# Kernel tuning notes

Hardware: AMD Instinct MI355X
Metric: run time of the kernel (lower is better)

Reference implementation:

```python
import jax, jax.numpy as jnp
import numpy as np

N_NODES = 16384   # total nodes
B = 32            # graphs in batch
NPG = 512         # nodes per graph (uniform -> dense mask is all True)
E = 262144        # edges (avg degree 16)
H = 64            # hidden_dim
HEADS = 8
DH = H // HEADS


def setup_inputs() -> dict:
    key = jax.random.key(0)
    ks = jax.random.split(key, 20)
    x = jax.random.normal(ks[0], (N_NODES, H), dtype=jnp.float32)
    # edges constrained within each graph of 512 nodes
    src = jax.random.randint(ks[1], (E,), 0, N_NODES, dtype=jnp.int32)
    dst = (src // NPG) * NPG + jax.random.randint(ks[2], (E,), 0, NPG, dtype=jnp.int32)
    edge_index = jnp.stack([src, dst])
    batch = (jnp.arange(N_NODES, dtype=jnp.int32) // NPG)
    c_size = jnp.full((B,), NPG, dtype=jnp.int32)
    s = 1.0 / np.sqrt(H)
    p = lambda k, shape: (jax.random.normal(k, shape, dtype=jnp.float32) * s)
    return {
        "x": x,
        "w_gat": p(ks[3], (H, H)), "att_src": p(ks[4], (H,)), "att_dst": p(ks[5], (H,)), "b_gat": jnp.zeros((H,), jnp.float32),
        "g1": jnp.ones((H,), jnp.float32), "b1": jnp.zeros((H,), jnp.float32),
        "wq": p(ks[6], (H, H)), "bq": jnp.zeros((H,), jnp.float32),
        "wk": p(ks[7], (H, H)), "bk": jnp.zeros((H,), jnp.float32),
        "wv": p(ks[8], (H, H)), "bv": jnp.zeros((H,), jnp.float32),
        "wo": p(ks[9], (H, H)), "bo": jnp.zeros((H,), jnp.float32),
        "g2": jnp.ones((H,), jnp.float32), "b2": jnp.zeros((H,), jnp.float32),
        "edge_index": edge_index, "batch": batch, "c_size": c_size,
    }


def _layer_norm(x, g, b):
    mu = jnp.mean(x, axis=-1, keepdims=True)
    var = jnp.var(x, axis=-1, keepdims=True)
    return (x - mu) * jax.lax.rsqrt(var + 1e-5) * g + b


def _gat_conv(x, edge_index, w, a_src, a_dst, bias):
    # PyG GATConv, 1 head, add_self_loops=True, leaky_relu slope 0.2
    n = x.shape[0]
    loops = jnp.arange(n, dtype=edge_index.dtype)
    src = jnp.concatenate([edge_index[0], loops])
    dst = jnp.concatenate([edge_index[1], loops])
    h = x @ w                                  # [n, H]
    e = jax.nn.leaky_relu((h @ a_src)[src] + (h @ a_dst)[dst], 0.2)  # [E+n]
    m = jax.ops.segment_max(e, dst, num_segments=n)
    p = jnp.exp(e - m[dst])
    s = jax.ops.segment_sum(p, dst, num_segments=n)
    alpha = p / (s[dst] + 1e-16)
    out = jax.ops.segment_sum(alpha[:, None] * h[src], dst, num_segments=n)
    return out + bias


def reference(x, w_gat, att_src, att_dst, b_gat, g1, b1,
              wq, bq, wk, bk, wv, bv, wo, bo, g2, b2,
              edge_index, batch, c_size):
    # GAT branch (dropout is identity in eval)
    x_ = jax.nn.relu(_gat_conv(x, edge_index, w_gat, att_src, att_dst, b_gat))
    x1 = _layer_norm(x + x_, g1, b1)                     # [n, H]
    # to_dense_batch: uniform graphs -> mask all True, plain reshape
    xd = x1.reshape(B, NPG, H)
    q = (xd @ wq + bq).reshape(B, NPG, HEADS, DH)
    k = (xd @ wk + bk).reshape(B, NPG, HEADS, DH)
    v = (xd @ wv + bv).reshape(B, NPG, HEADS, DH)
    scores = jnp.einsum('bqhd,bkhd->bhqk', q, k) / np.sqrt(DH)  # [B,h,N,N]
    attn = jax.nn.softmax(scores, axis=-1)
    o = jnp.einsum('bhqk,bkhd->bqhd', attn, v).reshape(B, NPG, H)
    o = o @ wo + bo
    x2 = _layer_norm(x1 + jax.nn.relu(o.reshape(N_NODES, H)), g2, b2)
    return x2  # recon_loss is None in eval mode
```

## Files before the change

### kernel.cpp

```cpp
#include <hip/hip_runtime.h>
#include <hip/hip_bf16.h>

#define NN     16384
#define HD     64
#define BG     32
#define NPG    512
#define NHEADS 8
#define DH     8
#define DEGMAX 40

#define KVSTR  20
#define CSTR   (64 * KVSTR + 4)
#define QSTR   12

typedef __hip_bfloat16 bf16;

#if defined(__has_builtin)
#if __has_builtin(__builtin_amdgcn_exp2f)
#define EXP2F(x) __builtin_amdgcn_exp2f(x)
#else
#define EXP2F(x) exp2f(x)
#endif
#else
#define EXP2F(x) exp2f(x)
#endif

__device__ __forceinline__ float b2f(bf16 v) { return __bfloat162float(v); }

__device__ __forceinline__ float ldf(const void* p, int i, int bf) {
  return bf ? __bfloat162float(((const bf16*)p)[i]) : ((const float*)p)[i];
}

__device__ __forceinline__ float wave_sum(float v) {
#pragma unroll
  for (int off = 32; off > 0; off >>= 1) v += __shfl_xor(v, off);
  return v;
}

__device__ __forceinline__ void unpack8(uint4 u, float* f) {
  f[0] = __uint_as_float(u.x << 16); f[1] = __uint_as_float(u.x & 0xffff0000u);
  f[2] = __uint_as_float(u.y << 16); f[3] = __uint_as_float(u.y & 0xffff0000u);
  f[4] = __uint_as_float(u.z << 16); f[5] = __uint_as_float(u.z & 0xffff0000u);
  f[6] = __uint_as_float(u.w << 16); f[7] = __uint_as_float(u.w & 0xffff0000u);
}

__device__ __forceinline__ unsigned short bfbits(float f) {
  bf16 b = __float2bfloat16(f);
  return *(unsigned short*)&b;
}

__device__ __forceinline__ int detect_bf(const unsigned short* xr, int tid, int nt) {
  __shared__ int s_cnt;
  if (tid == 0) s_cnt = 0;
  __syncthreads();
  int sane = 0;
  for (int i = tid; i < 256; i += nt) {
    int e = (xr[2 * i] >> 7) & 0xFF;
    sane += (e >= 100 && e <= 150) ? 1 : 0;
  }
  if (sane) atomicAdd(&s_cnt, sane);
  __syncthreads();
  return s_cnt > 180;
}

__global__ __launch_bounds__(256) void k_build(
    const void* __restrict__ x, const void* __restrict__ w,
    const void* __restrict__ asrc, const void* __restrict__ adst,
    const int* __restrict__ esrc, const int* __restrict__ edst, int E,
    int* __restrict__ cur, int* __restrict__ ell,
    bf16* __restrict__ h, float* __restrict__ as_, float* __restrict__ ad_,
    int* __restrict__ flagp)
{
  const int tid = threadIdx.x, lane = tid & 63, wid = tid >> 6;
  const int bf = detect_bf((const unsigned short*)x, tid, 256);
  if (tid == 0 && blockIdx.x == 0) *flagp = bf;
  __shared__ float wl[HD * HD];
  __shared__ float xr[4][HD];
  {
    for (int e = blockIdx.x * 256 + tid; e < E; e += gridDim.x * 256) {
      int d = edst[e];
      int k = atomicAdd(&cur[d], 1);
      if (k < DEGMAX) ell[d * DEGMAX + k] = esrc[e];
    }
  }
  for (int i = tid; i < HD * HD; i += 256) wl[i] = ldf(w, i, bf);
  const float av = ldf(asrc, lane, bf), dv_ = ldf(adst, lane, bf);
  __syncthreads();
#pragma unroll
  for (int r = 0; r < 4; ++r) {
    const int node = blockIdx.x * 16 + r * 4 + wid;
    xr[wid][lane] = ldf(x, node * HD + lane, bf);
    float hj = 0.f;
#pragma unroll
    for (int i = 0; i < HD; ++i) hj = fmaf(xr[wid][i], wl[i * HD + lane], hj);
    float pa = wave_sum(hj * av);
    float pd = wave_sum(hj * dv_);
    h[node * HD + lane] = __float2bfloat16(hj);
    if (lane == 0) { as_[node] = pa; ad_[node] = pd; }
  }
}

__global__ __launch_bounds__(256) void k_gather(
    const void* __restrict__ x, const int* __restrict__ cur,
    const int* __restrict__ ell, const float* __restrict__ as_,
    const float* __restrict__ ad_, const bf16* __restrict__ h,
    const void* __restrict__ bg, const void* __restrict__ g1,
    const void* __restrict__ b1, const int* __restrict__ dflag,
    bf16* __restrict__ x1)
{
  const int tid = threadIdx.x, lane = tid & 63, wid = tid >> 6;
  const int bf = *dflag;
  const int n = blockIdx.x * 4 + wid;
  const float adn = ad_[n];
  float e0 = as_[n] + adn;
  e0 = e0 > 0.f ? e0 : 0.2f * e0;
  float den = __expf(fminf(e0, 30.f));
  float num = den * b2f(h[n * HD + lane]);
  const int deg = min(cur[n], DEGMAX);
  const int* row = ell + n * DEGMAX;
  int i = 0;
  for (; i + 8 <= deg; i += 8) {
    int s[8];
#pragma unroll
    for (int k = 0; k < 8; ++k) s[k] = row[i + k];
    float a[8], hh[8];
#pragma unroll
    for (int k = 0; k < 8; ++k) a[k] = as_[s[k]];
#pragma unroll
    for (int k = 0; k < 8; ++k) hh[k] = b2f(h[s[k] * HD + lane]);
#pragma unroll
    for (int k = 0; k < 8; ++k) {
      float e = a[k] + adn;
      e = e > 0.f ? e : 0.2f * e;
      float p = __expf(fminf(e, 30.f));
      den += p;
      num = fmaf(p, hh[k], num);
    }
  }
  for (; i + 4 <= deg; i += 4) {
    int s0 = row[i], s1 = row[i + 1], s2 = row[i + 2], s3 = row[i + 3];
    float a0 = as_[s0], a1 = as_[s1], a2 = as_[s2], a3 = as_[s3];
    float h0 = b2f(h[s0 * HD + lane]), h1 = b2f(h[s1 * HD + lane]);
    float h2 = b2f(h[s2 * HD + lane]), h3 = b2f(h[s3 * HD + lane]);
    float e_0 = a0 + adn; e_0 = e_0 > 0.f ? e_0 : 0.2f * e_0;
    float e_1 = a1 + adn; e_1 = e_1 > 0.f ? e_1 : 0.2f * e_1;
    float e_2 = a2 + adn; e_2 = e_2 > 0.f ? e_2 : 0.2f * e_2;
    float e_3 = a3 + adn; e_3 = e_3 > 0.f ? e_3 : 0.2f * e_3;
    float p0 = __expf(fminf(e_0, 30.f)), p1 = __expf(fminf(e_1, 30.f));
    float p2 = __expf(fminf(e_2, 30.f)), p3 = __expf(fminf(e_3, 30.f));
    den += p0 + p1 + p2 + p3;
    num = fmaf(p0, h0, num); num = fmaf(p1, h1, num);
    num = fmaf(p2, h2, num); num = fmaf(p3, h3, num);
  }
  for (; i < deg; ++i) {
    int s = row[i];
    float e = as_[s] + adn;
    e = e > 0.f ? e : 0.2f * e;
    float p = __expf(fminf(e, 30.f));
    den += p;
    num = fmaf(p, b2f(h[s * HD + lane]), num);
  }
  float v = num / (den + 1e-16f) + ldf(bg, lane, bf);
  v = fmaxf(v, 0.f) + ldf(x, n * HD + lane, bf);
  float mu = wave_sum(v) * (1.f / 64.f);
  float dv = v - mu;
  float var = wave_sum(dv * dv) * (1.f / 64.f);
  float r = rsqrtf(var + 1e-5f);
  x1[n * HD + lane] =
      __float2bfloat16(dv * r * ldf(g1, lane, bf) + ldf(b1, lane, bf));
}

__global__ __launch_bounds__(256, 4) void k_attn13(
    const bf16* __restrict__ x1,
    const void* __restrict__ wq, const void* __restrict__ bq,
    const void* __restrict__ wk, const void* __restrict__ bk,
    const void* __restrict__ wv, const void* __restrict__ bv,
    const int* __restrict__ dflag,
    bf16* __restrict__ num_t, float* __restrict__ den_t)
{
  const int t = threadIdx.x;
  const int bf = *dflag;
  __shared__ float KV[4 * CSTR];
  __shared__ float Q[NPG * QSTR];
  __shared__ float Wl[3][HD][DH];
  __shared__ float bl[3][DH];
  const int bid = blockIdx.x;
  const int g = bid >> 4, hd = (bid >> 1) & 7, half = bid & 1;
  {
#pragma unroll
    for (int rr = 0; rr < 2; ++rr) {
      int idx = rr * 256 + t;
      int i = idx >> 3, j = idx & 7;
      int col = hd * DH + j;
      Wl[0][i][j] = ldf(wq, i * HD + col, bf);
      Wl[1][i][j] = ldf(wk, i * HD + col, bf);
      Wl[2][i][j] = ldf(wv, i * HD + col, bf);
    }
    if (t < DH) {
      bl[0][t] = ldf(bq, hd * DH + t, bf);
      bl[1][t] = ldf(bk, hd * DH + t, bf);
      bl[2][t] = ldf(bv, hd * DH + t, bf);
    }
  }
  __syncthreads();
  const float qscale = 0.3535533905932738f * 1.4426950408889634f;
  {
    const uint4* xk4 = (const uint4*)(x1 + (size_t)(g * NPG + half * 256 + t) * HD);
    float kr[DH], vr[DH];
#pragma unroll
    for (int j = 0; j < DH; ++j) { kr[j] = bl[1][j]; vr[j] = bl[2][j]; }
#pragma unroll
    for (int blk = 0; blk < 8; ++blk) {
      float xv[8];
      unpack8(xk4[blk], xv);
      const int ib = blk * 8;
#pragma unroll
      for (int ii = 0; ii < 8; ++ii)
#pragma unroll
        for (int j = 0; j < DH; ++j) {
          kr[j] = fmaf(xv[ii], Wl[1][ib + ii][j], kr[j]);
          vr[j] = fmaf(xv[ii], Wl[2][ib + ii][j], vr[j]);
        }
    }
    float* kvrow = KV + (t >> 6) * CSTR + (t & 63) * KVSTR;
    *(float4*)(kvrow +  0) = make_float4(kr[0], kr[1], kr[2], kr[3]);
    *(float4*)(kvrow +  4) = make_float4(kr[4], kr[5], kr[6], kr[7]);
    *(float4*)(kvrow +  8) = make_float4(vr[0], vr[1], vr[2], vr[3]);
    *(float4*)(kvrow + 12) = make_float4(vr[4], vr[5], vr[6], vr[7]);
  }
  {
    const uint4* xa4 = (const uint4*)(x1 + (size_t)(g * NPG + t) * HD);
    const uint4* xb4 = (const uint4*)(x1 + (size_t)(g * NPG + t + 256) * HD);
    float qa[DH], qb[DH];
#pragma unroll
    for (int j = 0; j < DH; ++j) { qa[j] = bl[0][j]; qb[j] = bl[0][j]; }
#pragma unroll
    for (int blk = 0; blk < 8; ++blk) {
      float xva[8], xvb[8];
      unpack8(xa4[blk], xva);
      unpack8(xb4[blk], xvb);
      const int ib = blk * 8;
#pragma unroll
      for (int ii = 0; ii < 8; ++ii)
#pragma unroll
        for (int j = 0; j < DH; ++j) {
          qa[j] = fmaf(xva[ii], Wl[0][ib + ii][j], qa[j]);
          qb[j] = fmaf(xvb[ii], Wl[0][ib + ii][j], qb[j]);
        }
    }
    float* q0 = Q + t * QSTR;
    float* q1 = Q + (t + 256) * QSTR;
    *(float4*)(q0 + 0) = make_float4(qa[0] * qscale, qa[1] * qscale, qa[2] * qscale, qa[3] * qscale);
    *(float4*)(q0 + 4) = make_float4(qa[4] * qscale, qa[5] * qscale, qa[6] * qscale, qa[7] * qscale);
    *(float4*)(q1 + 0) = make_float4(qb[0] * qscale, qb[1] * qscale, qb[2] * qscale, qb[3] * qscale);
    *(float4*)(q1 + 4) = make_float4(qb[4] * qscale, qb[5] * qscale, qb[6] * qscale, qb[7] * qscale);
  }
  __syncthreads();
  const int qg = t >> 2, c = t & 3;
  float qv[8][DH];
#pragma unroll
  for (int i = 0; i < 8; ++i) {
    const float* qrow = Q + (qg * 8 + i) * QSTR;
    float4 a = *(const float4*)(qrow);
    float4 b = *(const float4*)(qrow + 4);
    qv[i][0] = a.x; qv[i][1] = a.y; qv[i][2] = a.z; qv[i][3] = a.w;
    qv[i][4] = b.x; qv[i][5] = b.y; qv[i][6] = b.z; qv[i][7] = b.w;
  }
  float den[8], num[8][DH];
#pragma unroll
  for (int i = 0; i < 8; ++i) {
    den[i] = 0.f;
#pragma unroll
    for (int j = 0; j < DH; ++j) num[i][j] = 0.f;
  }
  const float* kvc = KV + c * CSTR;
  for (int jj = 0; jj < 64; ++jj) {
    const float4* kv4 = (const float4*)(kvc + jj * KVSTR);
    float4 k0 = kv4[0], k1 = kv4[1], v0 = kv4[2], v1 = kv4[3];
#pragma unroll
    for (int i = 0; i < 8; ++i) {
      float s = qv[i][0] * k0.x;
      s = fmaf(qv[i][1], k0.y, s); s = fmaf(qv[i][2], k0.z, s);
      s = fmaf(qv[i][3], k0.w, s); s = fmaf(qv[i][4], k1.x, s);
      s = fmaf(qv[i][5], k1.y, s); s = fmaf(qv[i][6], k1.z, s);
      s = fmaf(qv[i][7], k1.w, s);
      float p = EXP2F(s);
      den[i] += p;
      num[i][0] = fmaf(p, v0.x, num[i][0]); num[i][1] = fmaf(p, v0.y, num[i][1]);
      num[i][2] = fmaf(p, v0.z, num[i][2]); num[i][3] = fmaf(p, v0.w, num[i][3]);
      num[i][4] = fmaf(p, v1.x, num[i][4]); num[i][5] = fmaf(p, v1.y, num[i][5]);
      num[i][6] = fmaf(p, v1.z, num[i][6]); num[i][7] = fmaf(p, v1.w, num[i][7]);
    }
  }
#pragma unroll
  for (int st = 1; st <= 2; st <<= 1) {
#pragma unroll
    for (int i = 0; i < 8; ++i) {
      den[i] += __shfl_xor(den[i], st);
#pragma unroll
      for (int j = 0; j < DH; ++j) num[i][j] += __shfl_xor(num[i][j], st);
    }
  }
  const int plane = half * 8 + hd;
#pragma unroll
  for (int q2 = 0; q2 < 2; ++q2) {
    const int qi = 2 * c + q2;
    float dsel = 0.f, rsel[DH];
#pragma unroll
    for (int j = 0; j < DH; ++j) rsel[j] = 0.f;
#pragma unroll
    for (int i = 0; i < 8; ++i) {
      if (qi == i) {
        dsel = den[i];
#pragma unroll
        for (int j = 0; j < DH; ++j) rsel[j] = num[i][j];
      }
    }
    const int qrow = qg * 8 + qi;
    union { uint4 u4; unsigned short us[8]; } pk;
#pragma unroll
    for (int j = 0; j < DH; ++j) pk.us[j] = bfbits(rsel[j]);
    *(uint4*)(num_t + ((size_t)plane * NN + g * NPG + qrow) * 8) = pk.u4;
    den_t[(size_t)plane * NN + g * NPG + qrow] = dsel;
  }
}

__global__ __launch_bounds__(256) void k_out(
    const bf16* __restrict__ num_t, const float* __restrict__ den_t,
    const bf16* __restrict__ x1,
    const void* __restrict__ wo, const void* __restrict__ bo,
    const void* __restrict__ g2, const void* __restrict__ b2,
    const int* __restrict__ dflag, void* __restrict__ out)
{
  const int tid = threadIdx.x, lane = tid & 63, wid = tid >> 6;
  const int bf = *dflag;
  __shared__ float wl[HD * HD];
  __shared__ float orow[4][HD];
  for (int i = tid; i < HD * HD; i += 256) wl[i] = ldf(wo, i, bf);
  const float bov = ldf(bo, lane, bf);
  const float g2v = ldf(g2, lane, bf);
  const float b2v = ldf(b2, lane, bf);
  const int hdp = lane >> 3, jp = lane & 7;
  __syncthreads();
#pragma unroll
  for (int r = 0; r < 8; ++r) {
    const int node = blockIdx.x * 32 + r * 4 + wid;
    {
      float nm = b2f(num_t[((size_t)hdp * NN + node) * 8 + jp]) +
                 b2f(num_t[((size_t)(8 + hdp) * NN + node) * 8 + jp]);
      float dn = den_t[(size_t)hdp * NN + node] +
                 den_t[(size_t)(8 + hdp) * NN + node];
      orow[wid][lane] = nm / dn;
    }
    float y = bov;
#pragma unroll
    for (int i = 0; i < HD; ++i) y = fmaf(orow[wid][i], wl[i * HD + lane], y);
    float tt = b2f(x1[node * HD + lane]) + fmaxf(y, 0.f);
    float mu = wave_sum(tt) * (1.f / 64.f);
    float dv = tt - mu;
    float var = wave_sum(dv * dv) * (1.f / 64.f);
    float rr = rsqrtf(var + 1e-5f);
    float res = dv * rr * g2v + b2v;
    if (bf) ((bf16*)out)[node * HD + lane] = __float2bfloat16(res);
    else    ((float*)out)[node * HD + lane] = res;
  }
}

extern "C" void kernel_launch(void* const* d_in, const int* in_sizes, int n_in,
                              void* d_out, int out_size, void* d_ws, size_t ws_size,
                              hipStream_t stream)
{
  const void* x    = d_in[0];
  const void* wgat = d_in[1];
  const void* asrc = d_in[2];
  const void* adst = d_in[3];
  const void* bgat = d_in[4];
  const void* g1   = d_in[5];
  const void* b1   = d_in[6];
  const void* wq   = d_in[7];
  const void* bq   = d_in[8];
  const void* wk   = d_in[9];
  const void* bk   = d_in[10];
  const void* wv   = d_in[11];
  const void* bv   = d_in[12];
  const void* wo   = d_in[13];
  const void* bo   = d_in[14];
  const void* g2   = d_in[15];
  const void* b2   = d_in[16];
  const int*  ei   = (const int*)d_in[17];
  const int E = in_sizes[17] / 2;
  const int* esrc = ei;
  const int* edst = ei + E;

  char* W = (char*)d_ws;
  bf16*  x1b   = (bf16*)W;
  int*   ell   = (int*)(W + (size_t)(2 << 20));
  bf16*  hb    = (bf16*)(W + (size_t)(2 << 20) + (size_t)NN * DEGMAX * 4);
  bf16*  num_t = (bf16*)(W + (size_t)(2 << 20));
  float* den_t = (float*)(W + (size_t)(6 << 20));
  float* as_   = (float*)(W + (size_t)(7 << 20));
  float* ad_   = as_ + NN;
  int*   cur   = (int*)(ad_ + NN);
  int*   flag  = cur + NN;

  hipMemsetAsync(cur, 0, NN * sizeof(int), stream);
  k_build  <<<NN / 16, 256, 0, stream>>>(x, wgat, asrc, adst, esrc, edst, E,
                                         cur, ell, hb, as_, ad_, flag);
  k_gather <<<NN / 4, 256, 0, stream>>>(x, cur, ell, as_, ad_, hb,
                                        bgat, g1, b1, flag, x1b);
  k_attn13 <<<BG * NHEADS * 2, 256, 0, stream>>>(x1b, wq, bq, wk, bk, wv, bv,
                                                 flag, num_t, den_t);
  k_out    <<<NN / 32, 256, 0, stream>>>(num_t, den_t, x1b, wo, bo, g2, b2,
                                         flag, d_out);
}
```

Before: 200.4 us.

## Double attention kernel block size to halve per-thread query and KV work

```diff
diff --git a/kernel.cpp b/kernel.cpp
--- a/kernel.cpp
+++ b/kernel.cpp
@@ -170,7 +170,7 @@
       __float2bfloat16(dv * r * ldf(g1, lane, bf) + ldf(b1, lane, bf));
 }
 
-__global__ __launch_bounds__(256, 4) void k_attn13(
+__global__ __launch_bounds__(512, 4) void k_attn13(
     const bf16* __restrict__ x1,
     const void* __restrict__ wq, const void* __restrict__ bq,
     const void* __restrict__ wk, const void* __restrict__ bk,
@@ -187,15 +187,11 @@
   const int bid = blockIdx.x;
   const int g = bid >> 4, hd = (bid >> 1) & 7, half = bid & 1;
   {
-#pragma unroll
-    for (int rr = 0; rr < 2; ++rr) {
-      int idx = rr * 256 + t;
-      int i = idx >> 3, j = idx & 7;
-      int col = hd * DH + j;
-      Wl[0][i][j] = ldf(wq, i * HD + col, bf);
-      Wl[1][i][j] = ldf(wk, i * HD + col, bf);
-      Wl[2][i][j] = ldf(wv, i * HD + col, bf);
-    }
+    int i = t >> 3, j = t & 7;
+    int col = hd * DH + j;
+    Wl[0][i][j] = ldf(wq, i * HD + col, bf);
+    Wl[1][i][j] = ldf(wk, i * HD + col, bf);
+    Wl[2][i][j] = ldf(wv, i * HD + col, bf);
     if (t < DH) {
       bl[0][t] = ldf(bq, hd * DH + t, bf);
       bl[1][t] = ldf(bk, hd * DH + t, bf);
@@ -205,10 +201,12 @@
   __syncthreads();
   const float qscale = 0.3535533905932738f * 1.4426950408889634f;
   {
-    const uint4* xk4 = (const uint4*)(x1 + (size_t)(g * NPG + half * 256 + t) * HD);
-    float kr[DH], vr[DH];
-#pragma unroll
-    for (int j = 0; j < DH; ++j) { kr[j] = bl[1][j]; vr[j] = bl[2][j]; }
+    const int r = t & 255;
+    const int m = (t < 256) ? 1 : 2;
+    const uint4* xk4 = (const uint4*)(x1 + (size_t)(g * NPG + half * 256 + r) * HD);
+    float acc[DH];
+#pragma unroll
+    for (int j = 0; j < DH; ++j) acc[j] = bl[m][j];
 #pragma unroll
     for (int blk = 0; blk < 8; ++blk) {
       float xv[8];
@@ -217,58 +215,47 @@
 #pragma unroll
       for (int ii = 0; ii < 8; ++ii)
 #pragma unroll
-        for (int j = 0; j < DH; ++j) {
-          kr[j] = fmaf(xv[ii], Wl[1][ib + ii][j], kr[j]);
-          vr[j] = fmaf(xv[ii], Wl[2][ib + ii][j], vr[j]);
-        }
-    }
-    float* kvrow = KV + (t >> 6) * CSTR + (t & 63) * KVSTR;
-    *(float4*)(kvrow +  0) = make_float4(kr[0], kr[1], kr[2], kr[3]);
-    *(float4*)(kvrow +  4) = make_float4(kr[4], kr[5], kr[6], kr[7]);
-    *(float4*)(kvrow +  8) = make_float4(vr[0], vr[1], vr[2], vr[3]);
-    *(float4*)(kvrow + 12) = make_float4(vr[4], vr[5], vr[6], vr[7]);
+        for (int j = 0; j < DH; ++j)
+          acc[j] = fmaf(xv[ii], Wl[m][ib + ii][j], acc[j]);
+    }
+    float* kvrow = KV + (r >> 6) * CSTR + (r & 63) * KVSTR + (t < 256 ? 0 : 8);
+    *(float4*)(kvrow + 0) = make_float4(acc[0], acc[1], acc[2], acc[3]);
+    *(float4*)(kvrow + 4) = make_float4(acc[4], acc[5], acc[6], acc[7]);
   }
   {
     const uint4* xa4 = (const uint4*)(x1 + (size_t)(g * NPG + t) * HD);
-    const uint4* xb4 = (const uint4*)(x1 + (size_t)(g * NPG + t + 256) * HD);
-    float qa[DH], qb[DH];
-#pragma unroll
-    for (int j = 0; j < DH; ++j) { qa[j] = bl[0][j]; qb[j] = bl[0][j]; }
+    float qa[DH];
+#pragma unroll
+    for (int j = 0; j < DH; ++j) qa[j] = bl[0][j];
 #pragma unroll
     for (int blk = 0; blk < 8; ++blk) {
-      float xva[8], xvb[8];
-      unpack8(xa4[blk], xva);
-      unpack8(xb4[blk], xvb);
+      float xv[8];
+      unpack8(xa4[blk], xv);
       const int ib = blk * 8;
 #pragma unroll
       for (int ii = 0; ii < 8; ++ii)
 #pragma unroll
-        for (int j = 0; j < DH; ++j) {
-          qa[j] = fmaf(xva[ii], Wl[0][ib + ii][j], qa[j]);
-          qb[j] = fmaf(xvb[ii], Wl[0][ib + ii][j], qb[j]);
-        }
+        for (int j = 0; j < DH; ++j)
+          qa[j] = fmaf(xv[ii], Wl[0][ib + ii][j], qa[j]);
     }
     float* q0 = Q + t * QSTR;
-    float* q1 = Q + (t + 256) * QSTR;
     *(float4*)(q0 + 0) = make_float4(qa[0] * qscale, qa[1] * qscale, qa[2] * qscale, qa[3] * qscale);
     *(float4*)(q0 + 4) = make_float4(qa[4] * qscale, qa[5] * qscale, qa[6] * qscale, qa[7] * qscale);
-    *(float4*)(q1 + 0) = make_float4(qb[0] * qscale, qb[1] * qscale, qb[2] * qscale, qb[3] * qscale);
-    *(float4*)(q1 + 4) = make_float4(qb[4] * qscale, qb[5] * qscale, qb[6] * qscale, qb[7] * qscale);
   }
   __syncthreads();
   const int qg = t >> 2, c = t & 3;
-  float qv[8][DH];
-#pragma unroll
-  for (int i = 0; i < 8; ++i) {
-    const float* qrow = Q + (qg * 8 + i) * QSTR;
+  float qv[4][DH];
+#pragma unroll
+  for (int i = 0; i < 4; ++i) {
+    const float* qrow = Q + (qg * 4 + i) * QSTR;
     float4 a = *(const float4*)(qrow);
     float4 b = *(const float4*)(qrow + 4);
     qv[i][0] = a.x; qv[i][1] = a.y; qv[i][2] = a.z; qv[i][3] = a.w;
     qv[i][4] = b.x; qv[i][5] = b.y; qv[i][6] = b.z; qv[i][7] = b.w;
   }
-  float den[8], num[8][DH];
-#pragma unroll
-  for (int i = 0; i < 8; ++i) {
+  float den[4], num[4][DH];
+#pragma unroll
+  for (int i = 0; i < 4; ++i) {
     den[i] = 0.f;
 #pragma unroll
     for (int j = 0; j < DH; ++j) num[i][j] = 0.f;
@@ -278,7 +265,7 @@
     const float4* kv4 = (const float4*)(kvc + jj * KVSTR);
     float4 k0 = kv4[0], k1 = kv4[1], v0 = kv4[2], v1 = kv4[3];
 #pragma unroll
-    for (int i = 0; i < 8; ++i) {
+    for (int i = 0; i < 4; ++i) {
       float s = qv[i][0] * k0.x;
       s = fmaf(qv[i][1], k0.y, s); s = fmaf(qv[i][2], k0.z, s);
       s = fmaf(qv[i][3], k0.w, s); s = fmaf(qv[i][4], k1.x, s);
@@ -295,34 +282,30 @@
 #pragma unroll
   for (int st = 1; st <= 2; st <<= 1) {
 #pragma unroll
-    for (int i = 0; i < 8; ++i) {
+    for (int i = 0; i < 4; ++i) {
       den[i] += __shfl_xor(den[i], st);
 #pragma unroll
       for (int j = 0; j < DH; ++j) num[i][j] += __shfl_xor(num[i][j], st);
     }
   }
   const int plane = half * 8 + hd;
-#pragma unroll
-  for (int q2 = 0; q2 < 2; ++q2) {
-    const int qi = 2 * c + q2;
-    float dsel = 0.f, rsel[DH];
-#pragma unroll
-    for (int j = 0; j < DH; ++j) rsel[j] = 0.f;
-#pragma unroll
-    for (int i = 0; i < 8; ++i) {
-      if (qi == i) {
-        dsel = den[i];
-#pragma unroll
-        for (int j = 0; j < DH; ++j) rsel[j] = num[i][j];
-      }
-    }
-    const int qrow = qg * 8 + qi;
-    union { uint4 u4; unsigned short us[8]; } pk;
-#pragma unroll
-    for (int j = 0; j < DH; ++j) pk.us[j] = bfbits(rsel[j]);
-    *(uint4*)(num_t + ((size_t)plane * NN + g * NPG + qrow) * 8) = pk.u4;
-    den_t[(size_t)plane * NN + g * NPG + qrow] = dsel;
-  }
+  float dsel = 0.f, rsel[DH];
+#pragma unroll
+  for (int j = 0; j < DH; ++j) rsel[j] = 0.f;
+#pragma unroll
+  for (int i = 0; i < 4; ++i) {
+    if (c == i) {
+      dsel = den[i];
+#pragma unroll
+      for (int j = 0; j < DH; ++j) rsel[j] = num[i][j];
+    }
+  }
+  const int qrow = qg * 4 + c;
+  union { uint4 u4; unsigned short us[8]; } pk;
+#pragma unroll
+  for (int j = 0; j < DH; ++j) pk.us[j] = bfbits(rsel[j]);
+  *(uint4*)(num_t + ((size_t)plane * NN + g * NPG + qrow) * 8) = pk.u4;
+  den_t[(size_t)plane * NN + g * NPG + qrow] = dsel;
 }
 
 __global__ __launch_bounds__(256) void k_out(
@@ -408,7 +391,7 @@
                                          cur, ell, hb, as_, ad_, flag);
   k_gather <<<NN / 4, 256, 0, stream>>>(x, cur, ell, as_, ad_, hb,
                                         bgat, g1, b1, flag, x1b);
-  k_attn13 <<<BG * NHEADS * 2, 256, 0, stream>>>(x1b, wq, bq, wk, bk, wv, bv,
+  k_attn13 <<<BG * NHEADS * 2, 512, 0, stream>>>(x1b, wq, bq, wk, bk, wv, bv,
                                                  flag, num_t, den_t);
   k_out    <<<NN / 32, 256, 0, stream>>>(num_t, den_t, x1b, wo, bo, g2, b2,
                                          flag, d_out);
```

Result: faster. 195.6 us (-2.4%).
